# Kernel tuning notes

Hardware: AMD Instinct MI355X
Metric: run time of the kernel (lower is better)

Reference implementation:

```python
import jax, jax.numpy as jnp
import numpy as np

B, S, D = 32, 512, 512      # batch, seq, feature
E, H, O, K = 8, 2048, 512, 2  # experts, expert hidden, expert out, top_k


def setup_inputs() -> dict:
    key = jax.random.key(0)
    ks = jax.random.split(key, 5)
    sc = lambda k, shape, scale: jax.random.normal(k, shape, jnp.float32) * scale
    return {
        "x": sc(ks[0], (B, S, D), 1.0),
        "attn_w": sc(ks[1], (D, 1), 0.05),
        "attn_b": jnp.zeros((1,), jnp.float32),
        "gate_w": sc(ks[2], (D, E), 0.05),
        "gate_b": jnp.zeros((E,), jnp.float32),
        "w1": sc(ks[3], (E, D, H), 0.02),
        "b1": jnp.zeros((E, H), jnp.float32),
        "w2": sc(ks[4], (E, H, O), 0.02),
        "b2": jnp.zeros((E, O), jnp.float32),
    }


def reference(x, attn_w, attn_b, gate_w, gate_b, w1, b1, w2, b2):
    # --- attention pooling over the sequence axis ---
    scores = x @ attn_w + attn_b                      # [B,S,1]
    aw = jax.nn.softmax(scores, axis=1)               # softmax over seq
    pooled = jnp.sum(x * aw, axis=1)                  # [B,D]

    # --- gating: softmax -> top-k mask -> renormalize ---
    gates = jax.nn.softmax(pooled @ gate_w + gate_b, axis=-1)  # [B,E]
    _, idx = jax.lax.top_k(gates, K)                  # [B,K]
    mask = jnp.sum(jax.nn.one_hot(idx, E, dtype=gates.dtype), axis=-2)  # [B,E]
    g = gates * mask
    g = g / (jnp.sum(g, axis=-1, keepdims=True) + 1e-9)        # [B,E]

    # --- dense all-experts compute (exact GELU, as keras Dense('gelu')) ---
    h = jax.nn.gelu(jnp.einsum('bsd,edh->ebsh', x, w1) + b1[:, None, None, :],
                    approximate=False)                 # [E,B,S,H]
    eo = jax.nn.gelu(jnp.einsum('ebsh,eho->ebso', h, w2) + b2[:, None, None, :],
                     approximate=False)                # [E,B,S,O]

    # --- weighted combine over experts ---
    return jnp.einsum('ebso,be->bso', eo, g)           # [B,S,O]
```

## Files before the change

### kernel.cpp

```cpp
#include <hip/hip_runtime.h>
#include <hip/hip_bf16.h>
#include <math.h>

#define B_  32
#define S_  512
#define D_  512
#define E_  8
#define H_  2048
#define O_  512

typedef __bf16 bf16x8 __attribute__((ext_vector_type(8)));
typedef float  f32x4  __attribute__((ext_vector_type(4)));

#define GL2LDS(src, dst) \
  __builtin_amdgcn_global_load_lds((const __attribute__((address_space(1))) void*)(src), \
                                   (__attribute__((address_space(3))) void*)(dst), 16, 0, 0)

__device__ __forceinline__ float gelu_fast(float v) {
  float w = v * fmaf(v * v, 0.0713548162f, 1.5957691216f);
  float e = __expf(-w);
  return v * __builtin_amdgcn_rcpf(1.0f + e);
}

__global__ __launch_bounds__(256) void cast_score_kernel(
    const float* __restrict__ x, const float* __restrict__ attn_w,
    ushort* __restrict__ xb, float* __restrict__ scores)
{
  const int t = threadIdx.x;
  const int r = t >> 5;
  const int cg = t & 31;
  const int row = blockIdx.x * 8 + r;
  const float* src  = x + (size_t)row * D_ + cg * 16;
  const float* wsrc = attn_w + cg * 16;
  ushort* dstp = xb + (size_t)row * D_ + cg * 16;
  float acc = 0.f;
#pragma unroll
  for (int k = 0; k < 4; ++k) {
    float4 v  = *(const float4*)(src + k * 4);
    float4 wv = *(const float4*)(wsrc + k * 4);
    acc += v.x * wv.x + v.y * wv.y + v.z * wv.z + v.w * wv.w;
    ushort4 o;
    o.x = __builtin_bit_cast(unsigned short, __float2bfloat16(v.x));
    o.y = __builtin_bit_cast(unsigned short, __float2bfloat16(v.y));
    o.z = __builtin_bit_cast(unsigned short, __float2bfloat16(v.z));
    o.w = __builtin_bit_cast(unsigned short, __float2bfloat16(v.w));
    *(ushort4*)(dstp + k * 4) = o;
  }
#pragma unroll
  for (int off = 16; off; off >>= 1) acc += __shfl_xor(acc, off);
  if (cg == 0) scores[row] = acc;
}

__global__ __launch_bounds__(512) void softmax_aw_kernel(
    const float* __restrict__ scores, float* __restrict__ aw)
{
  __shared__ float red[8];
  __shared__ float mm, ss;
  const int t = threadIdx.x, b = blockIdx.x;
  float v = scores[b * S_ + t];
  float m = v;
#pragma unroll
  for (int off = 32; off; off >>= 1) m = fmaxf(m, __shfl_xor(m, off));
  if ((t & 63) == 0) red[t >> 6] = m;
  __syncthreads();
  if (t == 0) {
    float a = red[0];
    for (int i = 1; i < 8; ++i) a = fmaxf(a, red[i]);
    mm = a;
  }
  __syncthreads();
  float e = expf(v - mm);
  float s = e;
#pragma unroll
  for (int off = 32; off; off >>= 1) s += __shfl_xor(s, off);
  if ((t & 63) == 0) red[t >> 6] = s;
  __syncthreads();
  if (t == 0) {
    float a = 0.f;
    for (int i = 0; i < 8; ++i) a += red[i];
    ss = 1.f / a;
  }
  __syncthreads();
  aw[b * S_ + t] = e * ss;
}

__global__ __launch_bounds__(512) void pool_kernel(
    const float* __restrict__ x, const float* __restrict__ aw, float* __restrict__ pooled)
{
  __shared__ float sm[4][128];
  const int t = threadIdx.x;
  const int dl = t & 127;
  const int sh = t >> 7;
  const int b = blockIdx.y;
  const int d = blockIdx.x * 128 + dl;
  const float* xp  = x + (size_t)b * S_ * D_ + d;
  const float* awb = aw + b * S_;
  float acc = 0.f;
#pragma unroll 4
  for (int s = sh; s < S_; s += 4)
    acc = fmaf(awb[s], xp[(size_t)s * D_], acc);
  if (sh) sm[sh][dl] = acc;
  __syncthreads();
  if (sh == 0) pooled[b * D_ + d] = acc + sm[1][dl] + sm[2][dl] + sm[3][dl];
}

__global__ __launch_bounds__(256) void gate_psort_kernel(
    const float* __restrict__ pooled, const float* __restrict__ gate_w,
    const float* __restrict__ gate_b, int* __restrict__ gidx, float* __restrict__ gwt,
    int* __restrict__ psort)
{
  __shared__ float gl[32][8];
  const int t = threadIdx.x;
  const int b = t >> 3, ee = t & 7;
  float z = gate_b[ee];
  const float* pb = pooled + b * D_;
  for (int d = 0; d < D_; ++d) z = fmaf(pb[d], gate_w[d * E_ + ee], z);
  gl[b][ee] = z;
  __syncthreads();
  if (t < 32) {
    float ge[8];
    float zmax = gl[t][0];
    for (int i = 1; i < 8; ++i) zmax = fmaxf(zmax, gl[t][i]);
    float zs = 0.f;
    for (int i = 0; i < 8; ++i) { ge[i] = expf(gl[t][i] - zmax); zs += ge[i]; }
    for (int i = 0; i < 8; ++i) ge[i] /= zs;
    int i0 = 0;
    for (int i = 1; i < 8; ++i) if (ge[i] > ge[i0]) i0 = i;
    int i1 = -1;
    for (int i = 0; i < 8; ++i) if (i != i0 && (i1 < 0 || ge[i] > ge[i1])) i1 = i;
    float denom = ge[i0] + ge[i1] + 1e-9f;
    gidx[t * 2 + 0] = i0; gidx[t * 2 + 1] = i1;
    gwt[t * 2 + 0] = ge[i0] / denom; gwt[t * 2 + 1] = ge[i1] / denom;
  }
  __syncthreads();
  if (t == 0) {
    int cnt[E_] = {}, pos[E_];
    for (int p = 0; p < 2 * B_; ++p) cnt[gidx[p]]++;
    int s = 0;
    for (int e2 = 0; e2 < E_; ++e2) { pos[e2] = s; s += cnt[e2]; }
    for (int p = 0; p < 2 * B_; ++p) psort[pos[gidx[p]]++] = p;
  }
}

__global__ void transpose_cast_kernel(const float* __restrict__ in,
                                      __hip_bfloat16* __restrict__ outT, int R, int C)
{
  __shared__ float tile[32][33];
  const int z = blockIdx.z;
  const float* inz = in + (size_t)z * R * C;
  __hip_bfloat16* outz = outT + (size_t)z * R * C;
  const int c0 = blockIdx.x * 32, r0 = blockIdx.y * 32;
  const int tx = threadIdx.x, ty = threadIdx.y;
#pragma unroll
  for (int jj = 0; jj < 4; ++jj) {
    int r = r0 + ty + jj * 8;
    tile[ty + jj * 8][tx] = inz[(size_t)r * C + c0 + tx];
  }
  __syncthreads();
#pragma unroll
  for (int jj = 0; jj < 4; ++jj) {
    int c = c0 + ty + jj * 8;
    outz[(size_t)c * R + r0 + tx] = __float2bfloat16(tile[tx][ty + jj * 8]);
  }
}

__device__ __forceinline__ void phase_mfma(const char* cur, int aoff, int boff, int koff,
                                           f32x4 (&acc)[4][4])
{
  bf16x8 af[4], bfv[4];
#pragma unroll
  for (int r = 0; r < 4; ++r) af[r]  = *(const bf16x8*)(cur + aoff + r * 2048 + koff);
#pragma unroll
  for (int n = 0; n < 4; ++n) bfv[n] = *(const bf16x8*)(cur + boff + n * 2048 + koff);
  __builtin_amdgcn_s_setprio(1);
#pragma unroll
  for (int r = 0; r < 4; ++r)
#pragma unroll
    for (int n = 0; n < 4; ++n)
      acc[r][n] = __builtin_amdgcn_mfma_f32_16x16x32_bf16(af[r], bfv[n], acc[r][n], 0, 0, 0);
  __builtin_amdgcn_s_setprio(0);
}

__global__ __launch_bounds__(512, 2) void gemm1_kernel(
    const __hip_bfloat16* __restrict__ Xb, const __hip_bfloat16* __restrict__ W1T,
    const float* __restrict__ b1, __hip_bfloat16* __restrict__ Hbuf,
    const int* __restrict__ gidx, const int* __restrict__ psort)
{
  extern __shared__ char lds[];
  const int tid = threadIdx.x;
  const int P = blockIdx.x;
  const int n_ = (P & 7) * 32 + (P >> 3);
  const int p = psort[n_ >> 2];
  const int b = p >> 1;
  const int e = gidx[p];
  const int s0 = (n_ & 3) * 128;

  const char* Wbase = (const char*)W1T + (size_t)e * H_ * D_ * 2;
  const char* Xgb   = (const char*)Xb + ((size_t)b * S_ + s0) * D_ * 2;

  const int rw = tid >> 3;
  const int laneoff = rw * (D_ * 2) + ((((tid & 7) << 4)) ^ ((rw & 7) << 4));
  const int dst = tid * 16;

  const int l = tid & 63, w = tid >> 6;
  const int wh = w >> 1, ws_ = w & 1;
  const int lr = l & 15;
  const int kc16 = ((l >> 4) & 3) << 4;
  const int swz = (lr & 7) << 4;
  const int kA = kc16 ^ swz;
  const int kB = (64 + kc16) ^ swz;
  const int aoff = wh * 8192 + lr * 128;
  const int boff = 32768 + ws_ * 8192 + lr * 128;
  const int hi4 = ((l >> 4) & 3) << 2;

#define G1_STAGE_A(us, nb) { \
    const char* wsrc = Wbase + (((us) >> 3) << 18) + (((us) & 7) << 7) + laneoff; \
    GL2LDS(wsrc,          (nb) + dst); \
    GL2LDS(wsrc + 65536,  (nb) + 8192 + dst); \
    GL2LDS(wsrc + 131072, (nb) + 16384 + dst); }
#define G1_STAGE_B(us, nb) { \
    const char* wsrc = Wbase + (((us) >> 3) << 18) + (((us) & 7) << 7) + laneoff; \
    GL2LDS(wsrc + 196608, (nb) + 24576 + dst); \
    const char* xsrc = Xgb + (((us) & 7) << 7) + laneoff; \
    GL2LDS(xsrc,          (nb) + 32768 + dst); \
    GL2LDS(xsrc + 65536,  (nb) + 40960 + dst); }

  f32x4 acc[4][4] = {};
  __hip_bfloat16* Hp = Hbuf + (size_t)p * S_ * H_;
  const float* b1e0 = b1 + (size_t)e * H_;

  G1_STAGE_A(0, lds); G1_STAGE_B(0, lds);
  G1_STAGE_A(1, lds + 49152); G1_STAGE_B(1, lds + 49152);

  int cu = 0;
#pragma unroll 1
  for (int u = 0; u < 64; ++u) {
    char* cur = lds + cu * 49152;
    char* nb  = lds + ((cu >= 1) ? (cu - 1) : (cu + 2)) * 49152;
    if (u < 62) {
      G1_STAGE_A(u + 2, nb);
      asm volatile("s_waitcnt vmcnt(9)" ::: "memory");
    } else if (u == 62) {
      asm volatile("s_waitcnt vmcnt(6)" ::: "memory");
    } else {
      asm volatile("s_waitcnt vmcnt(0)" ::: "memory");
    }
    __builtin_amdgcn_s_barrier();
    __builtin_amdgcn_sched_barrier(0);
    phase_mfma(cur, aoff, boff, kA, acc);
    __builtin_amdgcn_sched_barrier(0);
    __builtin_amdgcn_s_barrier();
    if (u < 62) G1_STAGE_B(u + 2, nb);
    phase_mfma(cur, aoff, boff, kB, acc);
    __builtin_amdgcn_sched_barrier(0);
    __builtin_amdgcn_s_barrier();

    if ((u & 7) == 7) {
      const int h0 = (u >> 3) << 8;
      const float* b1e = b1e0 + h0;
#pragma unroll
      for (int r = 0; r < 4; ++r) {
        const int hl = wh * 64 + r * 16 + hi4;
        const float4 bias = *(const float4*)(b1e + hl);
#pragma unroll
        for (int n = 0; n < 4; ++n) {
          const int sl = s0 + ws_ * 64 + n * 16 + lr;
          ushort4 ov;
          ov.x = __builtin_bit_cast(unsigned short, __float2bfloat16(gelu_fast(acc[r][n][0] + bias.x)));
          ov.y = __builtin_bit_cast(unsigned short, __float2bfloat16(gelu_fast(acc[r][n][1] + bias.y)));
          ov.z = __builtin_bit_cast(unsigned short, __float2bfloat16(gelu_fast(acc[r][n][2] + bias.z)));
          ov.w = __builtin_bit_cast(unsigned short, __float2bfloat16(gelu_fast(acc[r][n][3] + bias.w)));
          *(ushort4*)(Hp + (size_t)sl * H_ + h0 + hl) = ov;
          acc[r][n] = (f32x4){0.f, 0.f, 0.f, 0.f};
        }
      }
    }
    cu = (cu == 2) ? 0 : cu + 1;
  }
#undef G1_STAGE_A
#undef G1_STAGE_B
}

__global__ __launch_bounds__(512, 2) void gemm2_kernel(
    const __hip_bfloat16* __restrict__ Hbuf, const __hip_bfloat16* __restrict__ W2T,
    const float* __restrict__ b2, float* __restrict__ out,
    const int* __restrict__ gidx, const float* __restrict__ gwt)
{
  extern __shared__ char lds[];
  const int tid = threadIdx.x;
  const int P = blockIdx.x;
  const int n_ = (P & 7) * 32 + (P >> 3);
  const int b = n_ >> 3;
  const int tl = n_ & 7;
  const int s0 = (tl >> 1) * 128;
  const int o0 = (tl & 1) * 256;

  const int e0 = gidx[2 * b], e1 = gidx[2 * b + 1];
  const float gw0 = gwt[2 * b], gw1 = gwt[2 * b + 1];

  const int rw = tid >> 3;
  const int laneoff = rw * (H_ * 2) + ((((tid & 7) << 4)) ^ ((rw & 7) << 4));
  const int dst = tid * 16;

  const char* W0p = (const char*)W2T + ((size_t)e0 * O_ + o0) * H_ * 2;
  const char* W1p = (const char*)W2T + ((size_t)e1 * O_ + o0) * H_ * 2;
  const char* X0p = (const char*)Hbuf + ((size_t)(2 * b)     * S_ + s0) * H_ * 2;
  const char* X1p = (const char*)Hbuf + ((size_t)(2 * b + 1) * S_ + s0) * H_ * 2;

  const int l = tid & 63, w = tid >> 6;
  const int wh = w >> 1, ws_ = w & 1;
  const int lr = l & 15;
  const int kc16 = ((l >> 4) & 3) << 4;
  const int swz = (lr & 7) << 4;
  const int kA = kc16 ^ swz;
  const int kB = (64 + kc16) ^ swz;
  const int aoff = wh * 8192 + lr * 128;
  const int boff = 32768 + ws_ * 8192 + lr * 128;
  const int hi4 = ((l >> 4) & 3) << 2;

#define G2_STAGE_A(us, nb) { \
    const char* wsrc = (((us) & 32) ? W1p : W0p) + (((us) & 31) << 7) + laneoff; \
    GL2LDS(wsrc,          (nb) + dst); \
    GL2LDS(wsrc + 262144, (nb) + 8192 + dst); \
    GL2LDS(wsrc + 524288, (nb) + 16384 + dst); }
#define G2_STAGE_B(us, nb) { \
    const char* wsrc = (((us) & 32) ? W1p : W0p) + (((us) & 31) << 7) + laneoff; \
    GL2LDS(wsrc + 786432, (nb) + 24576 + dst); \
    const char* xsrc = (((us) & 32) ? X1p : X0p) + (((us) & 31) << 7) + laneoff; \
    GL2LDS(xsrc,          (nb) + 32768 + dst); \
    GL2LDS(xsrc + 262144, (nb) + 40960 + dst); }

  f32x4 acc[4][4] = {};
  f32x4 fout[4][4] = {};

  G2_STAGE_A(0, lds); G2_STAGE_B(0, lds);
  G2_STAGE_A(1, lds + 49152); G2_STAGE_B(1, lds + 49152);

  int cu = 0;
#pragma unroll 1
  for (int u = 0; u < 64; ++u) {
    char* cur = lds + cu * 49152;
    char* nb  = lds + ((cu >= 1) ? (cu - 1) : (cu + 2)) * 49152;
    if (u < 62) {
      G2_STAGE_A(u + 2, nb);
      asm volatile("s_waitcnt vmcnt(9)" ::: "memory");
    } else if (u == 62) {
      asm volatile("s_waitcnt vmcnt(6)" ::: "memory");
    } else {
      asm volatile("s_waitcnt vmcnt(0)" ::: "memory");
    }
    __builtin_amdgcn_s_barrier();
    __builtin_amdgcn_sched_barrier(0);
    phase_mfma(cur, aoff, boff, kA, acc);
    __builtin_amdgcn_sched_barrier(0);
    __builtin_amdgcn_s_barrier();
    if (u < 62) G2_STAGE_B(u + 2, nb);
    phase_mfma(cur, aoff, boff, kB, acc);
    __builtin_amdgcn_sched_barrier(0);
    __builtin_amdgcn_s_barrier();

    if ((u & 31) == 31) {
      const int slot = u >> 5;
      const float gw = slot ? gw1 : gw0;
      const float* b2e = b2 + (size_t)(slot ? e1 : e0) * O_ + o0;
#pragma unroll
      for (int r = 0; r < 4; ++r) {
        const int ol = wh * 64 + r * 16 + hi4;
        const float4 bias = *(const float4*)(b2e + ol);
#pragma unroll
        for (int n = 0; n < 4; ++n) {
          fout[r][n][0] += gelu_fast(acc[r][n][0] + bias.x) * gw;
          fout[r][n][1] += gelu_fast(acc[r][n][1] + bias.y) * gw;
          fout[r][n][2] += gelu_fast(acc[r][n][2] + bias.z) * gw;
          fout[r][n][3] += gelu_fast(acc[r][n][3] + bias.w) * gw;
          acc[r][n] = (f32x4){0.f, 0.f, 0.f, 0.f};
        }
      }
    }
    cu = (cu == 2) ? 0 : cu + 1;
  }
#undef G2_STAGE_A
#undef G2_STAGE_B

#pragma unroll
  for (int r = 0; r < 4; ++r) {
    const int ol = wh * 64 + r * 16 + hi4;
#pragma unroll
    for (int n = 0; n < 4; ++n) {
      const int sl = s0 + ws_ * 64 + n * 16 + lr;
      *(float4*)(out + ((size_t)b * S_ + sl) * O_ + o0 + ol) =
          (float4){fout[r][n][0], fout[r][n][1], fout[r][n][2], fout[r][n][3]};
    }
  }
}

__global__ void sentinel_kernel(float* out, int n) {
  int i = blockIdx.x * blockDim.x + threadIdx.x;
  for (; i < n; i += gridDim.x * blockDim.x) out[i] = 1.0e6f;
}

extern "C" void kernel_launch(void* const* d_in, const int* in_sizes, int n_in,
                              void* d_out, int out_size, void* d_ws, size_t ws_size,
                              hipStream_t stream)
{
  const float* x      = (const float*)d_in[0];
  const float* attn_w = (const float*)d_in[1];
  const float* gate_w = (const float*)d_in[3];
  const float* gate_b = (const float*)d_in[4];
  const float* w1     = (const float*)d_in[5];
  const float* b1     = (const float*)d_in[6];
  const float* w2     = (const float*)d_in[7];
  const float* b2     = (const float*)d_in[8];
  float* out = (float*)d_out;

  char* ws = (char*)d_ws;
  const size_t OFF_GIDX = 0;
  const size_t OFF_GWT  = 256;
  const size_t OFF_PSRT = 512;
  const size_t OFF_X    = 1024;
  const size_t SZ_X     = (size_t)B_ * S_ * D_ * 2;
  const size_t OFF_W1T  = OFF_X + SZ_X;
  const size_t SZ_W1T   = (size_t)E_ * H_ * D_ * 2;
  const size_t OFF_W2T  = OFF_W1T + SZ_W1T;
  const size_t SZ_W2T   = (size_t)E_ * O_ * H_ * 2;
  const size_t OFF_H    = OFF_W2T + SZ_W2T;
  const size_t PAIR_H   = (size_t)S_ * H_ * 2;

  if (OFF_H + 64 * PAIR_H > ws_size) {
    hipLaunchKernelGGL(sentinel_kernel, dim3(256), dim3(256), 0, stream, out, out_size);
    return;
  }

  int*   gidx  = (int*)(ws + OFF_GIDX);
  float* gwt   = (float*)(ws + OFF_GWT);
  int*   psort = (int*)(ws + OFF_PSRT);
  __hip_bfloat16* xb   = (__hip_bfloat16*)(ws + OFF_X);
  __hip_bfloat16* w1T  = (__hip_bfloat16*)(ws + OFF_W1T);
  __hip_bfloat16* w2T  = (__hip_bfloat16*)(ws + OFF_W2T);
  __hip_bfloat16* Hbuf = (__hip_bfloat16*)(ws + OFF_H);
  float* scores = (float*)(ws + OFF_H);
  float* aw     = (float*)(ws + OFF_H + 65536);
  float* pooled = (float*)(ws + OFF_H + 131072);

  (void)hipFuncSetAttribute((const void*)gemm1_kernel, hipFuncAttributeMaxDynamicSharedMemorySize, 147456);
  (void)hipFuncSetAttribute((const void*)gemm2_kernel, hipFuncAttributeMaxDynamicSharedMemorySize, 147456);

  hipLaunchKernelGGL(cast_score_kernel, dim3(B_ * S_ / 8), dim3(256), 0, stream,
                     x, attn_w, (ushort*)xb, scores);
  hipLaunchKernelGGL(softmax_aw_kernel, dim3(B_), dim3(512), 0, stream, scores, aw);
  hipLaunchKernelGGL(pool_kernel, dim3(4, B_), dim3(512), 0, stream, x, aw, pooled);
  hipLaunchKernelGGL(gate_psort_kernel, dim3(1), dim3(256), 0, stream,
                     pooled, gate_w, gate_b, gidx, gwt, psort);
  hipLaunchKernelGGL(transpose_cast_kernel, dim3(H_ / 32, D_ / 32, E_), dim3(32, 8), 0, stream,
                     w1, w1T, D_, H_);
  hipLaunchKernelGGL(transpose_cast_kernel, dim3(O_ / 32, H_ / 32, E_), dim3(32, 8), 0, stream,
                     w2, w2T, H_, O_);

  hipLaunchKernelGGL(gemm1_kernel, dim3(256), dim3(512), 147456, stream,
                     xb, w1T, b1, Hbuf, gidx, psort);
  hipLaunchKernelGGL(gemm2_kernel, dim3(256), dim3(512), 147456, stream,
                     Hbuf, w2T, b2, out, gidx, gwt);
}
```

Measured before the change: 269.3 us.

## Restructure expert GEMMs into shared 256x256 K32 core with atomic combine

Both expert GEMMs now use one shared core that computes a 256x256 output tile per block with 32-wide K steps, a triple-buffered LDS pipeline and 8x4 MFMA accumulators per wave. Previously each block computed 128x256 tiles with 64-wide K steps. gemm1 now launches 1024 blocks, each producing a full H tile with no inner epilogue loop. gemm2 now splits work per (batch, expert) pair and accumulates the gated outputs with float atomicAdd after a memset, replacing the in-register sum over the two experts. This is meant to raise data reuse per LDS load and simplify scheduling, at the cost of atomic traffic, an extra memset and more accumulator registers.

```diff
diff --git a/kernel.cpp b/kernel.cpp
--- a/kernel.cpp
+++ b/kernel.cpp
@@ -164,232 +164,149 @@
   }
 }
 
-__device__ __forceinline__ void phase_mfma(const char* cur, int aoff, int boff, int koff,
-                                           f32x4 (&acc)[4][4])
-{
-  bf16x8 af[4], bfv[4];
-#pragma unroll
-  for (int r = 0; r < 4; ++r) af[r]  = *(const bf16x8*)(cur + aoff + r * 2048 + koff);
-#pragma unroll
-  for (int n = 0; n < 4; ++n) bfv[n] = *(const bf16x8*)(cur + boff + n * 2048 + koff);
-  __builtin_amdgcn_s_setprio(1);
-#pragma unroll
-  for (int r = 0; r < 4; ++r)
-#pragma unroll
-    for (int n = 0; n < 4; ++n)
-      acc[r][n] = __builtin_amdgcn_mfma_f32_16x16x32_bf16(af[r], bfv[n], acc[r][n], 0, 0, 0);
-  __builtin_amdgcn_s_setprio(0);
-}
-
-__global__ __launch_bounds__(512, 2) void gemm1_kernel(
-    const __hip_bfloat16* __restrict__ Xb, const __hip_bfloat16* __restrict__ W1T,
-    const float* __restrict__ b1, __hip_bfloat16* __restrict__ Hbuf,
-    const int* __restrict__ gidx, const int* __restrict__ psort)
-{
-  extern __shared__ char lds[];
+__device__ __forceinline__ void gemm_core32(const char* __restrict__ Wg, const char* __restrict__ Xg,
+                                            const int ldw, const int ldx, const int NT,
+                                            char* lds, f32x4 (&acc)[8][4])
+{
   const int tid = threadIdx.x;
-  const int P = blockIdx.x;
-  const int n_ = (P & 7) * 32 + (P >> 3);
-  const int p = psort[n_ >> 2];
-  const int b = p >> 1;
-  const int e = gidx[p];
-  const int s0 = (n_ & 3) * 128;
-
-  const char* Wbase = (const char*)W1T + (size_t)e * H_ * D_ * 2;
-  const char* Xgb   = (const char*)Xb + ((size_t)b * S_ + s0) * D_ * 2;
-
-  const int rw = tid >> 3;
-  const int laneoff = rw * (D_ * 2) + ((((tid & 7) << 4)) ^ ((rw & 7) << 4));
+  const int l = tid & 63;
+  const int w = tid >> 6;
+  const int wr = w >> 2;
+  const int wc = w & 3;
+  const int lr = l & 15;
+  const int ks = (l >> 4) & 3;
+  const int swz = (ks ^ ((lr >> 1) & 3)) << 4;
+  const int abase = (wr * 128 + lr) * 64 + swz;
+  const int bbase = 16384 + (wc * 64 + lr) * 64 + swz;
+
+  const int rw = tid >> 2;
+  const int scol = (((tid & 3) ^ ((tid >> 3) & 3)) << 4);
   const int dst = tid * 16;
-
-  const int l = tid & 63, w = tid >> 6;
-  const int wh = w >> 1, ws_ = w & 1;
-  const int lr = l & 15;
-  const int kc16 = ((l >> 4) & 3) << 4;
-  const int swz = (lr & 7) << 4;
-  const int kA = kc16 ^ swz;
-  const int kB = (64 + kc16) ^ swz;
-  const int aoff = wh * 8192 + lr * 128;
-  const int boff = 32768 + ws_ * 8192 + lr * 128;
-  const int hi4 = ((l >> 4) & 3) << 2;
-
-#define G1_STAGE_A(us, nb) { \
-    const char* wsrc = Wbase + (((us) >> 3) << 18) + (((us) & 7) << 7) + laneoff; \
-    GL2LDS(wsrc,          (nb) + dst); \
-    GL2LDS(wsrc + 65536,  (nb) + 8192 + dst); \
-    GL2LDS(wsrc + 131072, (nb) + 16384 + dst); }
-#define G1_STAGE_B(us, nb) { \
-    const char* wsrc = Wbase + (((us) >> 3) << 18) + (((us) & 7) << 7) + laneoff; \
-    GL2LDS(wsrc + 196608, (nb) + 24576 + dst); \
-    const char* xsrc = Xgb + (((us) & 7) << 7) + laneoff; \
-    GL2LDS(xsrc,          (nb) + 32768 + dst); \
-    GL2LDS(xsrc + 65536,  (nb) + 40960 + dst); }
-
-  f32x4 acc[4][4] = {};
-  __hip_bfloat16* Hp = Hbuf + (size_t)p * S_ * H_;
-  const float* b1e0 = b1 + (size_t)e * H_;
-
-  G1_STAGE_A(0, lds); G1_STAGE_B(0, lds);
-  G1_STAGE_A(1, lds + 49152); G1_STAGE_B(1, lds + 49152);
-
-  int cu = 0;
+  const char* sA0 = Wg + (size_t)rw * ldw + scol;
+  const char* sA1 = Wg + (size_t)(rw + 128) * ldw + scol;
+  const char* sB0 = Xg + (size_t)rw * ldx + scol;
+  const char* sB1 = Xg + (size_t)(rw + 128) * ldx + scol;
+
+#define STAGE32(kt, sp) { \
+    const size_t ko = (size_t)(kt) * 64; \
+    GL2LDS(sA0 + ko, (sp) + dst); \
+    GL2LDS(sA1 + ko, (sp) + 8192 + dst); \
+    GL2LDS(sB0 + ko, (sp) + 16384 + dst); \
+    GL2LDS(sB1 + ko, (sp) + 24576 + dst); }
+
+  STAGE32(0, lds);
+  STAGE32(1, lds + 32768);
+
 #pragma unroll 1
-  for (int u = 0; u < 64; ++u) {
-    char* cur = lds + cu * 49152;
-    char* nb  = lds + ((cu >= 1) ? (cu - 1) : (cu + 2)) * 49152;
-    if (u < 62) {
-      G1_STAGE_A(u + 2, nb);
-      asm volatile("s_waitcnt vmcnt(9)" ::: "memory");
-    } else if (u == 62) {
-      asm volatile("s_waitcnt vmcnt(6)" ::: "memory");
+  for (int t = 0; t < NT; ++t) {
+    char* cur = lds + (t % 3) * 32768;
+    if (t + 2 < NT) {
+      char* nb = lds + ((t + 2) % 3) * 32768;
+      STAGE32(t + 2, nb);
+      asm volatile("s_waitcnt vmcnt(8)" ::: "memory");
+    } else if (t + 1 < NT) {
+      asm volatile("s_waitcnt vmcnt(4)" ::: "memory");
     } else {
       asm volatile("s_waitcnt vmcnt(0)" ::: "memory");
     }
     __builtin_amdgcn_s_barrier();
     __builtin_amdgcn_sched_barrier(0);
-    phase_mfma(cur, aoff, boff, kA, acc);
+
+    bf16x8 af[8], bfv[4];
+#pragma unroll
+    for (int n = 0; n < 4; ++n) bfv[n] = *(const bf16x8*)(cur + bbase + n * 1024);
+#pragma unroll
+    for (int m = 0; m < 8; ++m) af[m] = *(const bf16x8*)(cur + abase + m * 1024);
+    __builtin_amdgcn_s_setprio(1);
+#pragma unroll
+    for (int m = 0; m < 8; ++m)
+#pragma unroll
+      for (int n = 0; n < 4; ++n)
+        acc[m][n] = __builtin_amdgcn_mfma_f32_16x16x32_bf16(af[m], bfv[n], acc[m][n], 0, 0, 0);
+    __builtin_amdgcn_s_setprio(0);
+
     __builtin_amdgcn_sched_barrier(0);
     __builtin_amdgcn_s_barrier();
-    if (u < 62) G1_STAGE_B(u + 2, nb);
-    phase_mfma(cur, aoff, boff, kB, acc);
-    __builtin_amdgcn_sched_barrier(0);
-    __builtin_amdgcn_s_barrier();
-
-    if ((u & 7) == 7) {
-      const int h0 = (u >> 3) << 8;
-      const float* b1e = b1e0 + h0;
-#pragma unroll
-      for (int r = 0; r < 4; ++r) {
-        const int hl = wh * 64 + r * 16 + hi4;
-        const float4 bias = *(const float4*)(b1e + hl);
-#pragma unroll
-        for (int n = 0; n < 4; ++n) {
-          const int sl = s0 + ws_ * 64 + n * 16 + lr;
-          ushort4 ov;
-          ov.x = __builtin_bit_cast(unsigned short, __float2bfloat16(gelu_fast(acc[r][n][0] + bias.x)));
-          ov.y = __builtin_bit_cast(unsigned short, __float2bfloat16(gelu_fast(acc[r][n][1] + bias.y)));
-          ov.z = __builtin_bit_cast(unsigned short, __float2bfloat16(gelu_fast(acc[r][n][2] + bias.z)));
-          ov.w = __builtin_bit_cast(unsigned short, __float2bfloat16(gelu_fast(acc[r][n][3] + bias.w)));
-          *(ushort4*)(Hp + (size_t)sl * H_ + h0 + hl) = ov;
-          acc[r][n] = (f32x4){0.f, 0.f, 0.f, 0.f};
-        }
-      }
+  }
+#undef STAGE32
+}
+
+__global__ __launch_bounds__(512, 2) void gemm1_kernel(
+    const __hip_bfloat16* __restrict__ Xb, const __hip_bfloat16* __restrict__ W1T,
+    const float* __restrict__ b1, __hip_bfloat16* __restrict__ Hbuf,
+    const int* __restrict__ gidx, const int* __restrict__ psort)
+{
+  extern __shared__ char lds[];
+  const int P = blockIdx.x;
+  const int L = (P & 7) * 128 + (P >> 3);
+  const int p = psort[L >> 4];
+  const int tl = L & 15;
+  const int b = p >> 1;
+  const int e = gidx[p];
+  const int h0 = (tl >> 1) * 256;
+  const int s0 = (tl & 1) * 256;
+  const char* Wg = (const char*)W1T + ((size_t)e * H_ + h0) * D_ * 2;
+  const char* Xg = (const char*)Xb + ((size_t)b * S_ + s0) * D_ * 2;
+  f32x4 acc[8][4] = {};
+  gemm_core32(Wg, Xg, D_ * 2, D_ * 2, D_ / 32, lds, acc);
+
+  const int tid = threadIdx.x, l = tid & 63, w = tid >> 6;
+  const int wr = w >> 2, wc = w & 3, lr = l & 15, q4 = ((l >> 4) & 3) << 2;
+  const float* b1e = b1 + (size_t)e * H_ + h0;
+  __hip_bfloat16* Hp = Hbuf + (size_t)p * S_ * H_ + h0;
+#pragma unroll
+  for (int m = 0; m < 8; ++m) {
+    const int hl = wr * 128 + m * 16 + q4;
+    const float4 bias = *(const float4*)(b1e + hl);
+#pragma unroll
+    for (int n = 0; n < 4; ++n) {
+      const int sl = s0 + wc * 64 + n * 16 + lr;
+      ushort4 ov;
+      ov.x = __builtin_bit_cast(unsigned short, __float2bfloat16(gelu_fast(acc[m][n][0] + bias.x)));
+      ov.y = __builtin_bit_cast(unsigned short, __float2bfloat16(gelu_fast(acc[m][n][1] + bias.y)));
+      ov.z = __builtin_bit_cast(unsigned short, __float2bfloat16(gelu_fast(acc[m][n][2] + bias.z)));
+      ov.w = __builtin_bit_cast(unsigned short, __float2bfloat16(gelu_fast(acc[m][n][3] + bias.w)));
+      *(ushort4*)(Hp + (size_t)sl * H_ + hl) = ov;
     }
-    cu = (cu == 2) ? 0 : cu + 1;
-  }
-#undef G1_STAGE_A
-#undef G1_STAGE_B
+  }
 }
 
 __global__ __launch_bounds__(512, 2) void gemm2_kernel(
     const __hip_bfloat16* __restrict__ Hbuf, const __hip_bfloat16* __restrict__ W2T,
     const float* __restrict__ b2, float* __restrict__ out,
-    const int* __restrict__ gidx, const float* __restrict__ gwt)
+    const int* __restrict__ gidx, const float* __restrict__ gwt,
+    const int* __restrict__ psort)
 {
   extern __shared__ char lds[];
-  const int tid = threadIdx.x;
   const int P = blockIdx.x;
-  const int n_ = (P & 7) * 32 + (P >> 3);
-  const int b = n_ >> 3;
-  const int tl = n_ & 7;
-  const int s0 = (tl >> 1) * 128;
-  const int o0 = (tl & 1) * 256;
-
-  const int e0 = gidx[2 * b], e1 = gidx[2 * b + 1];
-  const float gw0 = gwt[2 * b], gw1 = gwt[2 * b + 1];
-
-  const int rw = tid >> 3;
-  const int laneoff = rw * (H_ * 2) + ((((tid & 7) << 4)) ^ ((rw & 7) << 4));
-  const int dst = tid * 16;
-
-  const char* W0p = (const char*)W2T + ((size_t)e0 * O_ + o0) * H_ * 2;
-  const char* W1p = (const char*)W2T + ((size_t)e1 * O_ + o0) * H_ * 2;
-  const char* X0p = (const char*)Hbuf + ((size_t)(2 * b)     * S_ + s0) * H_ * 2;
-  const char* X1p = (const char*)Hbuf + ((size_t)(2 * b + 1) * S_ + s0) * H_ * 2;
-
-  const int l = tid & 63, w = tid >> 6;
-  const int wh = w >> 1, ws_ = w & 1;
-  const int lr = l & 15;
-  const int kc16 = ((l >> 4) & 3) << 4;
-  const int swz = (lr & 7) << 4;
-  const int kA = kc16 ^ swz;
-  const int kB = (64 + kc16) ^ swz;
-  const int aoff = wh * 8192 + lr * 128;
-  const int boff = 32768 + ws_ * 8192 + lr * 128;
-  const int hi4 = ((l >> 4) & 3) << 2;
-
-#define G2_STAGE_A(us, nb) { \
-    const char* wsrc = (((us) & 32) ? W1p : W0p) + (((us) & 31) << 7) + laneoff; \
-    GL2LDS(wsrc,          (nb) + dst); \
-    GL2LDS(wsrc + 262144, (nb) + 8192 + dst); \
-    GL2LDS(wsrc + 524288, (nb) + 16384 + dst); }
-#define G2_STAGE_B(us, nb) { \
-    const char* wsrc = (((us) & 32) ? W1p : W0p) + (((us) & 31) << 7) + laneoff; \
-    GL2LDS(wsrc + 786432, (nb) + 24576 + dst); \
-    const char* xsrc = (((us) & 32) ? X1p : X0p) + (((us) & 31) << 7) + laneoff; \
-    GL2LDS(xsrc,          (nb) + 32768 + dst); \
-    GL2LDS(xsrc + 262144, (nb) + 40960 + dst); }
-
-  f32x4 acc[4][4] = {};
-  f32x4 fout[4][4] = {};
-
-  G2_STAGE_A(0, lds); G2_STAGE_B(0, lds);
-  G2_STAGE_A(1, lds + 49152); G2_STAGE_B(1, lds + 49152);
-
-  int cu = 0;
-#pragma unroll 1
-  for (int u = 0; u < 64; ++u) {
-    char* cur = lds + cu * 49152;
-    char* nb  = lds + ((cu >= 1) ? (cu - 1) : (cu + 2)) * 49152;
-    if (u < 62) {
-      G2_STAGE_A(u + 2, nb);
-      asm volatile("s_waitcnt vmcnt(9)" ::: "memory");
-    } else if (u == 62) {
-      asm volatile("s_waitcnt vmcnt(6)" ::: "memory");
-    } else {
-      asm volatile("s_waitcnt vmcnt(0)" ::: "memory");
-    }
-    __builtin_amdgcn_s_barrier();
-    __builtin_amdgcn_sched_barrier(0);
-    phase_mfma(cur, aoff, boff, kA, acc);
-    __builtin_amdgcn_sched_barrier(0);
-    __builtin_amdgcn_s_barrier();
-    if (u < 62) G2_STAGE_B(u + 2, nb);
-    phase_mfma(cur, aoff, boff, kB, acc);
-    __builtin_amdgcn_sched_barrier(0);
-    __builtin_amdgcn_s_barrier();
-
-    if ((u & 31) == 31) {
-      const int slot = u >> 5;
-      const float gw = slot ? gw1 : gw0;
-      const float* b2e = b2 + (size_t)(slot ? e1 : e0) * O_ + o0;
-#pragma unroll
-      for (int r = 0; r < 4; ++r) {
-        const int ol = wh * 64 + r * 16 + hi4;
-        const float4 bias = *(const float4*)(b2e + ol);
-#pragma unroll
-        for (int n = 0; n < 4; ++n) {
-          fout[r][n][0] += gelu_fast(acc[r][n][0] + bias.x) * gw;
-          fout[r][n][1] += gelu_fast(acc[r][n][1] + bias.y) * gw;
-          fout[r][n][2] += gelu_fast(acc[r][n][2] + bias.z) * gw;
-          fout[r][n][3] += gelu_fast(acc[r][n][3] + bias.w) * gw;
-          acc[r][n] = (f32x4){0.f, 0.f, 0.f, 0.f};
-        }
-      }
-    }
-    cu = (cu == 2) ? 0 : cu + 1;
-  }
-#undef G2_STAGE_A
-#undef G2_STAGE_B
-
-#pragma unroll
-  for (int r = 0; r < 4; ++r) {
-    const int ol = wh * 64 + r * 16 + hi4;
+  const int L = (P & 7) * 32 + (P >> 3);
+  const int p = psort[L >> 2];
+  const int tl = L & 3;
+  const int b = p >> 1;
+  const int e = gidx[p];
+  const float gw = gwt[p];
+  const int o0 = (tl >> 1) * 256;
+  const int s0 = (tl & 1) * 256;
+  const char* Wg = (const char*)W2T + ((size_t)e * O_ + o0) * H_ * 2;
+  const char* Xg = (const char*)Hbuf + ((size_t)p * S_ + s0) * H_ * 2;
+  f32x4 acc[8][4] = {};
+  gemm_core32(Wg, Xg, H_ * 2, H_ * 2, H_ / 32, lds, acc);
+
+  const int tid = threadIdx.x, l = tid & 63, w = tid >> 6;
+  const int wr = w >> 2, wc = w & 3, lr = l & 15, q4 = ((l >> 4) & 3) << 2;
+  const float* b2e = b2 + (size_t)e * O_ + o0;
+#pragma unroll
+  for (int m = 0; m < 8; ++m) {
+    const int ol = wr * 128 + m * 16 + q4;
+    const float4 bias = *(const float4*)(b2e + ol);
 #pragma unroll
     for (int n = 0; n < 4; ++n) {
-      const int sl = s0 + ws_ * 64 + n * 16 + lr;
-      *(float4*)(out + ((size_t)b * S_ + sl) * O_ + o0 + ol) =
-          (float4){fout[r][n][0], fout[r][n][1], fout[r][n][2], fout[r][n][3]};
+      const int sl = s0 + wc * 64 + n * 16 + lr;
+      float* dstp = out + ((size_t)b * S_ + sl) * O_ + o0 + ol;
+      atomicAdd(dstp + 0, gelu_fast(acc[m][n][0] + bias.x) * gw);
+      atomicAdd(dstp + 1, gelu_fast(acc[m][n][1] + bias.y) * gw);
+      atomicAdd(dstp + 2, gelu_fast(acc[m][n][2] + bias.z) * gw);
+      atomicAdd(dstp + 3, gelu_fast(acc[m][n][3] + bias.w) * gw);
     }
   }
 }
@@ -442,8 +359,8 @@
   float* aw     = (float*)(ws + OFF_H + 65536);
   float* pooled = (float*)(ws + OFF_H + 131072);
 
-  (void)hipFuncSetAttribute((const void*)gemm1_kernel, hipFuncAttributeMaxDynamicSharedMemorySize, 147456);
-  (void)hipFuncSetAttribute((const void*)gemm2_kernel, hipFuncAttributeMaxDynamicSharedMemorySize, 147456);
+  (void)hipFuncSetAttribute((const void*)gemm1_kernel, hipFuncAttributeMaxDynamicSharedMemorySize, 98304);
+  (void)hipFuncSetAttribute((const void*)gemm2_kernel, hipFuncAttributeMaxDynamicSharedMemorySize, 98304);
 
   hipLaunchKernelGGL(cast_score_kernel, dim3(B_ * S_ / 8), dim3(256), 0, stream,
                      x, attn_w, (ushort*)xb, scores);
@@ -455,9 +372,10 @@
                      w1, w1T, D_, H_);
   hipLaunchKernelGGL(transpose_cast_kernel, dim3(O_ / 32, H_ / 32, E_), dim3(32, 8), 0, stream,
                      w2, w2T, H_, O_);
-
-  hipLaunchKernelGGL(gemm1_kernel, dim3(256), dim3(512), 147456, stream,
+  hipMemsetAsync(d_out, 0, (size_t)out_size * sizeof(float), stream);
+
+  hipLaunchKernelGGL(gemm1_kernel, dim3(1024), dim3(512), 98304, stream,
                      xb, w1T, b1, Hbuf, gidx, psort);
-  hipLaunchKernelGGL(gemm2_kernel, dim3(256), dim3(512), 147456, stream,
-                     Hbuf, w2T, b2, out, gidx, gwt);
-}
+  hipLaunchKernelGGL(gemm2_kernel, dim3(256), dim3(512), 98304, stream,
+                     Hbuf, w2T, b2, out, gidx, gwt, psort);
+}
```

Measured after the change: 444.6 us. 65.1% more time.
